# Performance work log

Measured on AMD Instinct MI355X. Metric: run time of the kernel, lower is better.

## Reference

```python
import jax, jax.numpy as jnp
import numpy as np

N_NODES = 40000
N_EDGES = 640000
N_FEAT = 128
HIDDEN = 128
N_GRAPHS = 64


def _sage_conv(x, src, dst, Wl, b, Wr):
    # PyG SAGEConv (aggr='mean', root_weight=True, normalize=False):
    # out_i = W_l @ mean_{j in N(i)} x_j + b + W_r @ x_i
    msg = x[src]                                             # [E, F]
    s = jax.ops.segment_sum(msg, dst, num_segments=N_NODES)  # [N, F]
    deg = jax.ops.segment_sum(jnp.ones((src.shape[0],), x.dtype), dst,
                              num_segments=N_NODES)
    agg = s / jnp.maximum(deg, 1.0)[:, None]
    return agg @ Wl + b + x @ Wr


def setup_inputs() -> dict:
    key = jax.random.key(0)
    ks = jax.random.split(key, 12)
    sc = 1.0 / np.sqrt(N_FEAT)
    x = jax.random.normal(ks[0], (N_NODES, N_FEAT), dtype=jnp.float32)
    edge_index = jax.random.randint(ks[1], (2, N_EDGES), 0, N_NODES, dtype=jnp.int32)
    batch = jnp.sort(jax.random.randint(ks[2], (N_NODES,), 0, N_GRAPHS, dtype=jnp.int32))
    mk = lambda k, shp: (jax.random.normal(k, shp, dtype=jnp.float32) * sc)
    return {
        'x': x, 'edge_index': edge_index, 'batch': batch,
        'W1l': mk(ks[3], (N_FEAT, HIDDEN)), 'b1': jnp.zeros((HIDDEN,), jnp.float32),
        'W1r': mk(ks[4], (N_FEAT, HIDDEN)),
        'W2l': mk(ks[5], (HIDDEN, HIDDEN)), 'b2': jnp.zeros((HIDDEN,), jnp.float32),
        'W2r': mk(ks[6], (HIDDEN, HIDDEN)),
        'W3l': mk(ks[7], (HIDDEN, HIDDEN)), 'b3': jnp.zeros((HIDDEN,), jnp.float32),
        'W3r': mk(ks[8], (HIDDEN, HIDDEN)),
        'Wlin': mk(ks[9], (3 * HIDDEN, HIDDEN)), 'blin': jnp.zeros((HIDDEN,), jnp.float32),
    }


def reference(x, edge_index, batch, W1l, b1, W1r, W2l, b2, W2r, W3l, b3, W3r, Wlin, blin):
    src, dst = edge_index[0], edge_index[1]
    h1 = jax.nn.relu(_sage_conv(x, src, dst, W1l, b1, W1r))
    h2 = jax.nn.relu(_sage_conv(h1, src, dst, W2l, b2, W2r))
    h3 = jax.nn.relu(_sage_conv(h2, src, dst, W3l, b3, W3r))
    h = jnp.concatenate([h1, h2, h3], axis=1)                # [N, 3*H]
    pooled = jax.ops.segment_sum(h, batch, num_segments=N_GRAPHS)  # global_add_pool
    out = jax.nn.relu(pooled @ Wlin + blin)                  # [G, H]
    return out
```

## Files before the change

kernel.cpp:

```cpp
#include <hip/hip_runtime.h>
#include <hip/hip_bf16.h>

#define N_NODES 40000
#define N_EDGES 640000
#define NFEAT 128
#define NGRAPHS 64
#define ECAP 1024


typedef __attribute__((ext_vector_type(8))) short short8;
typedef __attribute__((ext_vector_type(4))) float float4v;
typedef __attribute__((ext_vector_type(2))) float float2v;

static __device__ __forceinline__ unsigned short f2bf(float f) {
    unsigned int x = __builtin_bit_cast(unsigned int, f);
    unsigned int r = x + 0x7fffu + ((x >> 16) & 1u);
    return (unsigned short)(r >> 16);
}

__global__ void k_prep(const int* __restrict__ dst, int* __restrict__ deg,
                       const float* __restrict__ x, unsigned short* __restrict__ h0,
                       const float* __restrict__ Wl0, const float* __restrict__ Wr0,
                       const float* __restrict__ Wl1, const float* __restrict__ Wr1,
                       const float* __restrict__ Wl2, const float* __restrict__ Wr2,
                       unsigned short* __restrict__ Wt, float* __restrict__ pooled) {
    int b = blockIdx.x;
    if (b < 625) {
        int e0 = b * 1024 + threadIdx.x;
        #pragma unroll
        for (int k = 0; k < 4; ++k) {
            int e = e0 + k * 256;
            if (e < N_EDGES) atomicAdd(&deg[dst[e]], 1);
        }
    } else if (b < 1875) {
        const int n = N_NODES * NFEAT / 8;
        int i0 = (b - 625) * 512 + threadIdx.x;
        const float4* xf = (const float4*)x;
        #pragma unroll
        for (int k = 0; k < 2; ++k) {
            int i = i0 + k * 256;
            if (i < n) {
                float4 p0 = xf[2 * i], p1 = xf[2 * i + 1];
                uint4 v;
                v.x = (unsigned int)f2bf(p0.x) | ((unsigned int)f2bf(p0.y) << 16);
                v.y = (unsigned int)f2bf(p0.z) | ((unsigned int)f2bf(p0.w) << 16);
                v.z = (unsigned int)f2bf(p1.x) | ((unsigned int)f2bf(p1.y) << 16);
                v.w = (unsigned int)f2bf(p1.z) | ((unsigned int)f2bf(p1.w) << 16);
                ((uint4*)h0)[i] = v;
            }
        }
    } else if (b < 2259) {
        int id = (b - 1875) * 256 + threadIdx.x;
        if (id >= 3 * 128 * 256) return;
        int l   = id >> 15;
        int rem = id & 32767;
        int nn  = rem >> 8;
        int k   = rem & 255;
        const float* Wl = (l == 0) ? Wl0 : (l == 1) ? Wl1 : Wl2;
        const float* Wr = (l == 0) ? Wr0 : (l == 1) ? Wr1 : Wr2;
        float v = (k < 128) ? Wl[k * 128 + nn] : Wr[(k - 128) * 128 + nn];
        Wt[id] = f2bf(v);
    } else {
        int j = (b - 2259) * 256 + threadIdx.x;
        if (j < NGRAPHS * 384) pooled[j] = 0.f;
    }
}

__global__ __launch_bounds__(1024) void k_scan(const int* __restrict__ deg,
                                               int* __restrict__ offsets,
                                               int* __restrict__ cursor) {
    __shared__ int ws[16];
    __shared__ int s_boff;
    int tid = threadIdx.x;
    int b = blockIdx.x;
    int lane = tid & 63, wave = tid >> 6;

    int lim = b << 10;
    int s = 0;
    for (int i = tid; i < lim; i += 1024) s += deg[i];
    for (int d = 1; d < 64; d <<= 1) s += __shfl_xor(s, d, 64);
    if (lane == 0) ws[wave] = s;
    __syncthreads();
    if (tid == 0) {
        int t = 0;
        for (int w = 0; w < 16; ++w) t += ws[w];
        s_boff = t;
    }
    __syncthreads();
    int boff = s_boff;

    int i = (b << 10) + tid;
    int v = (i < N_NODES) ? deg[i] : 0;
    int incl = v;
    for (int d = 1; d < 64; d <<= 1) {
        int t = __shfl_up(incl, d, 64);
        if (lane >= d) incl += t;
    }
    __syncthreads();
    if (lane == 63) ws[wave] = incl;
    __syncthreads();
    if (wave == 0 && lane < 16) {
        int w = ws[lane];
        for (int d = 1; d < 16; d <<= 1) {
            int t = __shfl_up(w, d, 64);
            if (lane >= d) w += t;
        }
        ws[lane] = w;
    }
    __syncthreads();
    int waveOff = (wave == 0) ? 0 : ws[wave - 1];
    if (i < N_NODES) {
        int o = boff + waveOff + incl - v;
        offsets[i] = o;
        cursor[i]  = o;
    }
    if (b == 39 && tid == 0) offsets[N_NODES] = N_EDGES;
}

__global__ void k_fill(const int* __restrict__ src, const int* __restrict__ dst,
                       int* __restrict__ cursor, unsigned short* __restrict__ esrc) {
    int e0 = blockIdx.x * 512 + threadIdx.x;
    #pragma unroll
    for (int k = 0; k < 2; ++k) {
        int e = e0 + k * 256;
        if (e < N_EDGES) {
            int d = dst[e];
            int p = atomicAdd(&cursor[d], 1);
            esrc[p] = (unsigned short)src[e];
        }
    }
}

__global__ __launch_bounds__(256, 8) void k_sage(
        const unsigned short* __restrict__ hin,
        const int* __restrict__ offsets,
        const unsigned short* __restrict__ esrc,
        const int* __restrict__ batch,
        const unsigned short* __restrict__ Wt,
        const float* __restrict__ bias,
        unsigned short* __restrict__ hout,
        float* __restrict__ poolseg) {
    __shared__ __align__(16) unsigned short As[32][264];
    __shared__ __align__(16) unsigned short eidx[ECAP];
    int tid = threadIdx.x;
    int row0 = blockIdx.x * 32;

    int estart = offsets[row0];
    int ecnt   = offsets[row0 + 32] - estart;
    int staged = ecnt < ECAP ? ecnt : ECAP;

    for (int p = 0; p < 2; ++p) {
        int ci = tid + p * 256;
        int r = ci >> 4, c8 = ci & 15;
        uint4 v = *(const uint4*)(hin + (size_t)(row0 + r) * 128 + c8 * 8);
        *(uint4*)(&As[r][128 + c8 * 8]) = v;
    }
    for (int t = tid; t < staged; t += 256) eidx[t] = esrc[estart + t];
    __syncthreads();

    {
        int grp = tid >> 4;
        int sub = tid & 15;
        for (int nn = 0; nn < 2; ++nn) {
            int r = nn * 16 + grp;
            int node = row0 + r;
            int beg = offsets[node], end = offsets[node + 1];
            float2v a0 = {0.f, 0.f}, a1 = a0, a2 = a0, a3 = a0;
            auto acc8 = [&](uint4 u) {
                float2v t0, t1, t2, t3;
                t0.x = __builtin_bit_cast(float, u.x << 16);
                t0.y = __builtin_bit_cast(float, u.x & 0xffff0000u);
                t1.x = __builtin_bit_cast(float, u.y << 16);
                t1.y = __builtin_bit_cast(float, u.y & 0xffff0000u);
                t2.x = __builtin_bit_cast(float, u.z << 16);
                t2.y = __builtin_bit_cast(float, u.z & 0xffff0000u);
                t3.x = __builtin_bit_cast(float, u.w << 16);
                t3.y = __builtin_bit_cast(float, u.w & 0xffff0000u);
                a0 += t0; a1 += t1; a2 += t2; a3 += t3;
            };
            if (end - estart <= staged) {
                int lj = beg - estart, lend = end - estart;
                for (; lj + 8 <= lend; lj += 8) {
                    int s0 = eidx[lj],     s1 = eidx[lj + 1];
                    int s2 = eidx[lj + 2], s3 = eidx[lj + 3];
                    int s4 = eidx[lj + 4], s5 = eidx[lj + 5];
                    int s6 = eidx[lj + 6], s7 = eidx[lj + 7];
                    uint4 u0 = *(const uint4*)(hin + (size_t)s0 * 128 + sub * 8);
                    uint4 u1 = *(const uint4*)(hin + (size_t)s1 * 128 + sub * 8);
                    uint4 u2 = *(const uint4*)(hin + (size_t)s2 * 128 + sub * 8);
                    uint4 u3 = *(const uint4*)(hin + (size_t)s3 * 128 + sub * 8);
                    uint4 u4 = *(const uint4*)(hin + (size_t)s4 * 128 + sub * 8);
                    uint4 u5 = *(const uint4*)(hin + (size_t)s5 * 128 + sub * 8);
                    uint4 u6 = *(const uint4*)(hin + (size_t)s6 * 128 + sub * 8);
                    uint4 u7 = *(const uint4*)(hin + (size_t)s7 * 128 + sub * 8);
                    acc8(u0); acc8(u1); acc8(u2); acc8(u3);
                    acc8(u4); acc8(u5); acc8(u6); acc8(u7);
                }
                for (; lj < lend; ++lj) {
                    int s = eidx[lj];
                    uint4 u = *(const uint4*)(hin + (size_t)s * 128 + sub * 8);
                    acc8(u);
                }
            } else {
                for (int j = beg; j < end; ++j) {
                    int s = esrc[j];
                    uint4 u = *(const uint4*)(hin + (size_t)s * 128 + sub * 8);
                    acc8(u);
                }
            }
            int deg = end - beg;
            float inv = 1.f / (float)(deg > 1 ? deg : 1);
            uint4 v;
            v.x = (unsigned int)f2bf(a0.x * inv) | ((unsigned int)f2bf(a0.y * inv) << 16);
            v.y = (unsigned int)f2bf(a1.x * inv) | ((unsigned int)f2bf(a1.y * inv) << 16);
            v.z = (unsigned int)f2bf(a2.x * inv) | ((unsigned int)f2bf(a2.y * inv) << 16);
            v.w = (unsigned int)f2bf(a3.x * inv) | ((unsigned int)f2bf(a3.y * inv) << 16);
            *(uint4*)(&As[r][sub * 8]) = v;
        }
    }
    __syncthreads();

    int wave = tid >> 6, lane = tid & 63;
    int quad = lane >> 4, l16 = lane & 15;
    float4v acc[2][2];
    for (int rt = 0; rt < 2; ++rt)
        for (int ct = 0; ct < 2; ++ct) acc[rt][ct] = {0.f, 0.f, 0.f, 0.f};

    int ncol0 = wave * 32;
    for (int kc = 0; kc < 8; ++kc) {
        int k0 = kc * 32 + quad * 8;
        short8 a[2], b[2];
        for (int rt = 0; rt < 2; ++rt)
            a[rt] = *(const short8*)(&As[rt * 16 + l16][k0]);
        for (int ct = 0; ct < 2; ++ct)
            b[ct] = *(const short8*)(Wt + (size_t)(ncol0 + ct * 16 + l16) * 256 + k0);
        for (int rt = 0; rt < 2; ++rt)
            for (int ct = 0; ct < 2; ++ct)
                acc[rt][ct] = __builtin_amdgcn_mfma_f32_16x16x32_bf16(
                    a[rt], b[ct], acc[rt][ct], 0, 0, 0);
    }

    __syncthreads();
    float* Ps = (float*)&As[0][0];
    int* sbatch = (int*)&eidx[0];
    if (tid < 32) sbatch[tid] = batch[row0 + tid];

    for (int ct = 0; ct < 2; ++ct) {
        int col = ncol0 + ct * 16 + l16;
        float bv = bias[col];
        for (int rt = 0; rt < 2; ++rt) {
            int r0 = rt * 16 + quad * 4;
            for (int i = 0; i < 4; ++i) {
                float v = acc[rt][ct][i] + bv;
                v = v > 0.f ? v : 0.f;
                if (hout) hout[(size_t)(row0 + r0 + i) * 128 + col] = f2bf(v);
                Ps[(r0 + i) * 132 + col] = v;
            }
        }
    }
    __syncthreads();

    {
        int half = tid >> 7;
        int c = tid & 127;
        int rbase = half * 16;
        float accp = 0.f;
        int cur = sbatch[rbase];
        for (int r = rbase; r < rbase + 16; ++r) {
            int g = sbatch[r];
            if (g != cur) {
                atomicAdd(&poolseg[cur * 384 + c], accp);
                accp = 0.f;
                cur = g;
            }
            accp += Ps[r * 132 + c];
        }
        atomicAdd(&poolseg[cur * 384 + c], accp);
    }
}

__global__ void k_final(const float* __restrict__ pooled,
                        const float* __restrict__ Wlin,
                        const float* __restrict__ blin,
                        float* __restrict__ out) {
    __shared__ float part[128];
    int g = blockIdx.x;
    int t = threadIdx.x;
    int col = t & 127, half = t >> 7;
    int k0 = half * 192;
    float acc = 0.f;
    for (int k = k0; k < k0 + 192; ++k)
        acc = fmaf(pooled[g * 384 + k], Wlin[k * 128 + col], acc);
    if (half) part[col] = acc;
    __syncthreads();
    if (!half) {
        float v = acc + part[col] + blin[col];
        out[g * 128 + col] = v > 0.f ? v : 0.f;
    }
}

extern "C" void kernel_launch(void* const* d_in, const int* in_sizes, int n_in,
                              void* d_out, int out_size, void* d_ws, size_t ws_size,
                              hipStream_t stream) {
    const float* x    = (const float*)d_in[0];
    const int*   ei   = (const int*)d_in[1];
    const int*   src  = ei;
    const int*   dst  = ei + N_EDGES;
    const int*   batch = (const int*)d_in[2];
    const float* W1l = (const float*)d_in[3];
    const float* b1  = (const float*)d_in[4];
    const float* W1r = (const float*)d_in[5];
    const float* W2l = (const float*)d_in[6];
    const float* b2  = (const float*)d_in[7];
    const float* W2r = (const float*)d_in[8];
    const float* W3l = (const float*)d_in[9];
    const float* b3  = (const float*)d_in[10];
    const float* W3r = (const float*)d_in[11];
    const float* Wlin = (const float*)d_in[12];
    const float* blin = (const float*)d_in[13];
    float* out = (float*)d_out;

    char* ws = (char*)d_ws;
    size_t off = 0;
    auto alloc = [&](size_t bytes) -> char* {
        char* p = ws + off;
        off = (off + bytes + 255) & ~(size_t)255;
        return p;
    };
    int* offsets = (int*)alloc((N_NODES + 1) * sizeof(int));
    int* cursor  = (int*)alloc(N_NODES * sizeof(int));
    int* deg     = (int*)alloc(N_NODES * sizeof(int));
    unsigned short* esrc = (unsigned short*)alloc(N_EDGES * sizeof(unsigned short));
    unsigned short* h0   = (unsigned short*)alloc((size_t)N_NODES * 128 * 2);
    unsigned short* h1   = (unsigned short*)alloc((size_t)N_NODES * 128 * 2);
    unsigned short* h2   = (unsigned short*)alloc((size_t)N_NODES * 128 * 2);
    unsigned short* Wt   = (unsigned short*)alloc(3 * 256 * 128 * 2);
    float* pooled = (float*)alloc(NGRAPHS * 384 * sizeof(float));

    hipMemsetAsync(deg, 0, N_NODES * sizeof(int), stream);

    k_prep<<<2355, 256, 0, stream>>>(dst, deg, x, h0,
                                     W1l, W1r, W2l, W2r, W3l, W3r, Wt, pooled);
    k_scan<<<40, 1024, 0, stream>>>(deg, offsets, cursor);
    k_fill<<<1250, 256, 0, stream>>>(src, dst, cursor, esrc);

    k_sage<<<1250, 256, 0, stream>>>(h0, offsets, esrc, batch, Wt,
                                     b1, h1, pooled);
    k_sage<<<1250, 256, 0, stream>>>(h1, offsets, esrc, batch, Wt + 32768,
                                     b2, h2, pooled + 128);
    k_sage<<<1250, 256, 0, stream>>>(h2, offsets, esrc, batch, Wt + 2 * 32768,
                                     b3, (unsigned short*)nullptr, pooled + 256);

    k_final<<<NGRAPHS, 256, 0, stream>>>(pooled, Wlin, blin, out);
}
```

Measured before the change: 257.1 us.

## Double-buffer neighbor gathers with masked 8-wide batches in SAGE aggregation

Restructures the neighbor-mean gather loop so two 8-edge batches are kept in flight at once: the next batch's loads are issued before the current batch is accumulated. Tails are handled by clamping indices and masking with a 0/1 multiplier via FMA, which removes the scalar remainder loop. Launch bounds are relaxed from 8 to 4 blocks per SM to give room for the extra registers the two 8-wide uint4 buffers need. The trade-off is lower occupancy and some redundant loads on tail batches, in exchange for more memory-level parallelism per thread.

```diff
diff --git a/kernel.cpp b/kernel.cpp
--- a/kernel.cpp
+++ b/kernel.cpp
@@ -131,7 +131,7 @@
     }
 }
 
-__global__ __launch_bounds__(256, 8) void k_sage(
+__global__ __launch_bounds__(256, 4) void k_sage(
         const unsigned short* __restrict__ hin,
         const int* __restrict__ offsets,
         const unsigned short* __restrict__ esrc,
@@ -161,12 +161,14 @@
     {
         int grp = tid >> 4;
         int sub = tid & 15;
+        const unsigned short* hsub = hin + sub * 8;
         for (int nn = 0; nn < 2; ++nn) {
             int r = nn * 16 + grp;
             int node = row0 + r;
             int beg = offsets[node], end = offsets[node + 1];
             float2v a0 = {0.f, 0.f}, a1 = a0, a2 = a0, a3 = a0;
-            auto acc8 = [&](uint4 u) {
+            auto acc1 = [&](uint4 u, float m) {
+                float2v mv = {m, m};
                 float2v t0, t1, t2, t3;
                 t0.x = __builtin_bit_cast(float, u.x << 16);
                 t0.y = __builtin_bit_cast(float, u.x & 0xffff0000u);
@@ -176,36 +178,65 @@
                 t2.y = __builtin_bit_cast(float, u.z & 0xffff0000u);
                 t3.x = __builtin_bit_cast(float, u.w << 16);
                 t3.y = __builtin_bit_cast(float, u.w & 0xffff0000u);
-                a0 += t0; a1 += t1; a2 += t2; a3 += t3;
+                a0 = t0 * mv + a0;
+                a1 = t1 * mv + a1;
+                a2 = t2 * mv + a2;
+                a3 = t3 * mv + a3;
+            };
+            auto accb = [&](const uint4* U, int rem) {
+                #pragma unroll
+                for (int i = 0; i < 8; ++i)
+                    acc1(U[i], i < rem ? 1.f : 0.f);
             };
             if (end - estart <= staged) {
                 int lj = beg - estart, lend = end - estart;
-                for (; lj + 8 <= lend; lj += 8) {
-                    int s0 = eidx[lj],     s1 = eidx[lj + 1];
-                    int s2 = eidx[lj + 2], s3 = eidx[lj + 3];
-                    int s4 = eidx[lj + 4], s5 = eidx[lj + 5];
-                    int s6 = eidx[lj + 6], s7 = eidx[lj + 7];
-                    uint4 u0 = *(const uint4*)(hin + (size_t)s0 * 128 + sub * 8);
-                    uint4 u1 = *(const uint4*)(hin + (size_t)s1 * 128 + sub * 8);
-                    uint4 u2 = *(const uint4*)(hin + (size_t)s2 * 128 + sub * 8);
-                    uint4 u3 = *(const uint4*)(hin + (size_t)s3 * 128 + sub * 8);
-                    uint4 u4 = *(const uint4*)(hin + (size_t)s4 * 128 + sub * 8);
-                    uint4 u5 = *(const uint4*)(hin + (size_t)s5 * 128 + sub * 8);
-                    uint4 u6 = *(const uint4*)(hin + (size_t)s6 * 128 + sub * 8);
-                    uint4 u7 = *(const uint4*)(hin + (size_t)s7 * 128 + sub * 8);
-                    acc8(u0); acc8(u1); acc8(u2); acc8(u3);
-                    acc8(u4); acc8(u5); acc8(u6); acc8(u7);
-                }
-                for (; lj < lend; ++lj) {
-                    int s = eidx[lj];
-                    uint4 u = *(const uint4*)(hin + (size_t)s * 128 + sub * 8);
-                    acc8(u);
+                int len = lend - lj;
+                if (len > 0) {
+                    int jmax = lend - 1;
+                    auto issue = [&](int base, uint4* U) {
+                        #pragma unroll
+                        for (int i = 0; i < 8; ++i) {
+                            int j = base + i;
+                            j = j <= jmax ? j : jmax;
+                            int s = eidx[j];
+                            U[i] = *(const uint4*)(hsub + (size_t)s * 128);
+                        }
+                    };
+                    uint4 U[8], V[8];
+                    issue(lj, U);
+                    int remU = len;
+                    int b = lj + 8;
+                    while (b < lend) {
+                        issue(b, V);
+                        accb(U, remU);
+                        int remV = lend - b;
+                        b += 8;
+                        if (b < lend) {
+                            issue(b, U);
+                            accb(V, remV);
+                            remU = lend - b;
+                            b += 8;
+                        } else {
+                            accb(V, remV);
+                            remU = 0;
+                            break;
+                        }
+                    }
+                    if (remU > 0) accb(U, remU);
                 }
             } else {
-                for (int j = beg; j < end; ++j) {
-                    int s = esrc[j];
-                    uint4 u = *(const uint4*)(hin + (size_t)s * 128 + sub * 8);
-                    acc8(u);
+                int jmax = end - 1;
+                for (int j = beg; j < end; j += 8) {
+                    int rem = end - j;
+                    uint4 U[8];
+                    #pragma unroll
+                    for (int i = 0; i < 8; ++i) {
+                        int jj = j + i;
+                        jj = jj <= jmax ? jj : jmax;
+                        int s = esrc[jj];
+                        U[i] = *(const uint4*)(hsub + (size_t)s * 128);
+                    }
+                    accb(U, rem);
                 }
             }
             int deg = end - beg;
```

New measurement: 262.3 us. 1.02x slower.

## Stage neighbor rows into LDS with async double-buffered global_load_lds

Applied to the files above, without the earlier changes.

Replaces the per-thread register gather of neighbor feature rows with a block-cooperative, double-buffered pipeline. The whole block stages 64 edges' bf16 rows at a time into LDS using global_load_lds, while the previously staged chunk is accumulated from LDS. The goal is to keep many gather loads in flight and hide their latency. In exchange it adds about 32KB of LDS, two barriers per chunk, and some wasted loads (clamped slots at the tail). Occupancy is lowered (launch bounds 8→4), and nodes with skewed degrees now wait on each other at block barriers.

```diff
diff --git a/kernel.cpp b/kernel.cpp
--- a/kernel.cpp
+++ b/kernel.cpp
@@ -6,6 +6,7 @@
 #define NFEAT 128
 #define NGRAPHS 64
 #define ECAP 1024
+#define CHUNK 64
 
 
 typedef __attribute__((ext_vector_type(8))) short short8;
@@ -16,6 +17,13 @@
     unsigned int x = __builtin_bit_cast(unsigned int, f);
     unsigned int r = x + 0x7fffu + ((x >> 16) & 1u);
     return (unsigned short)(r >> 16);
+}
+
+static __device__ __forceinline__ void stage16(const unsigned short* g,
+                                               unsigned short* l) {
+    __builtin_amdgcn_global_load_lds(
+        (const __attribute__((address_space(1))) void*)g,
+        (__attribute__((address_space(3))) void*)l, 16, 0, 0);
 }
 
 __global__ void k_prep(const int* __restrict__ dst, int* __restrict__ deg,
@@ -131,7 +139,7 @@
     }
 }
 
-__global__ __launch_bounds__(256, 8) void k_sage(
+__global__ __launch_bounds__(256, 4) void k_sage(
         const unsigned short* __restrict__ hin,
         const int* __restrict__ offsets,
         const unsigned short* __restrict__ esrc,
@@ -141,13 +149,14 @@
         unsigned short* __restrict__ hout,
         float* __restrict__ poolseg) {
     __shared__ __align__(16) unsigned short As[32][264];
+    __shared__ __align__(16) unsigned short Ebuf[2][CHUNK * 128];
     __shared__ __align__(16) unsigned short eidx[ECAP];
     int tid = threadIdx.x;
     int row0 = blockIdx.x * 32;
 
     int estart = offsets[row0];
     int ecnt   = offsets[row0 + 32] - estart;
-    int staged = ecnt < ECAP ? ecnt : ECAP;
+    int SC = ecnt < ECAP ? ecnt : ECAP;
 
     for (int p = 0; p < 2; ++p) {
         int ci = tid + p * 256;
@@ -155,72 +164,114 @@
         uint4 v = *(const uint4*)(hin + (size_t)(row0 + r) * 128 + c8 * 8);
         *(uint4*)(&As[r][128 + c8 * 8]) = v;
     }
-    for (int t = tid; t < staged; t += 256) eidx[t] = esrc[estart + t];
-    __syncthreads();
-
+    for (int t = tid; t < SC; t += 256) eidx[t] = esrc[estart + t];
+    __syncthreads();
+
+    int lane = tid & 63, wave = tid >> 6;
+    int grp = tid >> 4, sub = tid & 15;
+
+    int beg0, end0, beg1, end1;
     {
-        int grp = tid >> 4;
-        int sub = tid & 15;
-        for (int nn = 0; nn < 2; ++nn) {
-            int r = nn * 16 + grp;
-            int node = row0 + r;
-            int beg = offsets[node], end = offsets[node + 1];
-            float2v a0 = {0.f, 0.f}, a1 = a0, a2 = a0, a3 = a0;
-            auto acc8 = [&](uint4 u) {
-                float2v t0, t1, t2, t3;
-                t0.x = __builtin_bit_cast(float, u.x << 16);
-                t0.y = __builtin_bit_cast(float, u.x & 0xffff0000u);
-                t1.x = __builtin_bit_cast(float, u.y << 16);
-                t1.y = __builtin_bit_cast(float, u.y & 0xffff0000u);
-                t2.x = __builtin_bit_cast(float, u.z << 16);
-                t2.y = __builtin_bit_cast(float, u.z & 0xffff0000u);
-                t3.x = __builtin_bit_cast(float, u.w << 16);
-                t3.y = __builtin_bit_cast(float, u.w & 0xffff0000u);
-                a0 += t0; a1 += t1; a2 += t2; a3 += t3;
-            };
-            if (end - estart <= staged) {
-                int lj = beg - estart, lend = end - estart;
-                for (; lj + 8 <= lend; lj += 8) {
-                    int s0 = eidx[lj],     s1 = eidx[lj + 1];
-                    int s2 = eidx[lj + 2], s3 = eidx[lj + 3];
-                    int s4 = eidx[lj + 4], s5 = eidx[lj + 5];
-                    int s6 = eidx[lj + 6], s7 = eidx[lj + 7];
-                    uint4 u0 = *(const uint4*)(hin + (size_t)s0 * 128 + sub * 8);
-                    uint4 u1 = *(const uint4*)(hin + (size_t)s1 * 128 + sub * 8);
-                    uint4 u2 = *(const uint4*)(hin + (size_t)s2 * 128 + sub * 8);
-                    uint4 u3 = *(const uint4*)(hin + (size_t)s3 * 128 + sub * 8);
-                    uint4 u4 = *(const uint4*)(hin + (size_t)s4 * 128 + sub * 8);
-                    uint4 u5 = *(const uint4*)(hin + (size_t)s5 * 128 + sub * 8);
-                    uint4 u6 = *(const uint4*)(hin + (size_t)s6 * 128 + sub * 8);
-                    uint4 u7 = *(const uint4*)(hin + (size_t)s7 * 128 + sub * 8);
-                    acc8(u0); acc8(u1); acc8(u2); acc8(u3);
-                    acc8(u4); acc8(u5); acc8(u6); acc8(u7);
-                }
-                for (; lj < lend; ++lj) {
-                    int s = eidx[lj];
-                    uint4 u = *(const uint4*)(hin + (size_t)s * 128 + sub * 8);
-                    acc8(u);
-                }
+        int n0 = row0 + grp,      n1 = row0 + 16 + grp;
+        beg0 = offsets[n0] - estart;  end0 = offsets[n0 + 1] - estart;
+        beg1 = offsets[n1] - estart;  end1 = offsets[n1 + 1] - estart;
+    }
+    float2v A0[4], A1[4];
+    #pragma unroll
+    for (int i = 0; i < 4; ++i) { A0[i] = {0.f, 0.f}; A1[i] = {0.f, 0.f}; }
+
+    auto addu = [&](uint4 u, float2v* A) {
+        float2v t0, t1, t2, t3;
+        t0.x = __builtin_bit_cast(float, u.x << 16);
+        t0.y = __builtin_bit_cast(float, u.x & 0xffff0000u);
+        t1.x = __builtin_bit_cast(float, u.y << 16);
+        t1.y = __builtin_bit_cast(float, u.y & 0xffff0000u);
+        t2.x = __builtin_bit_cast(float, u.z << 16);
+        t2.y = __builtin_bit_cast(float, u.z & 0xffff0000u);
+        t3.x = __builtin_bit_cast(float, u.w << 16);
+        t3.y = __builtin_bit_cast(float, u.w & 0xffff0000u);
+        A[0] += t0; A[1] += t1; A[2] += t2; A[3] += t3;
+    };
+
+    int nc = (SC + CHUNK - 1) >> 6;
+    if (nc > 0) {
+        auto stage_chunk = [&](int c, int par) {
+            int c0 = c << 6;
+            #pragma unroll
+            for (int i = 0; i < 4; ++i) {
+                int slot = wave * 4 + i;
+                int el = c0 + slot * 4 + (lane >> 4);
+                el = el < SC - 1 ? el : SC - 1;
+                int s = eidx[el];
+                const unsigned short* g = hin + (size_t)s * 128 + (lane & 15) * 8;
+                stage16(g, &Ebuf[par][slot * 512]);
+            }
+        };
+        auto accum_chunk = [&](int c, int par) {
+            int c0 = c << 6, c1 = c0 + CHUNK;
+            int lim = c1 < SC ? c1 : SC;
+            {
+                int lo = beg0 > c0 ? beg0 : c0;
+                int hi = end0 < lim ? end0 : lim;
+                for (int e = lo; e < hi; ++e)
+                    addu(*(const uint4*)&Ebuf[par][(e - c0) * 128 + sub * 8], A0);
+            }
+            {
+                int lo = beg1 > c0 ? beg1 : c0;
+                int hi = end1 < lim ? end1 : lim;
+                for (int e = lo; e < hi; ++e)
+                    addu(*(const uint4*)&Ebuf[par][(e - c0) * 128 + sub * 8], A1);
+            }
+        };
+
+        stage_chunk(0, 0);
+        for (int c = 0; c < nc; ++c) {
+            int par = c & 1;
+            if (c + 1 < nc) {
+                stage_chunk(c + 1, par ^ 1);
+                asm volatile("s_waitcnt vmcnt(4)" ::: "memory");
             } else {
-                for (int j = beg; j < end; ++j) {
-                    int s = esrc[j];
-                    uint4 u = *(const uint4*)(hin + (size_t)s * 128 + sub * 8);
-                    acc8(u);
-                }
-            }
-            int deg = end - beg;
-            float inv = 1.f / (float)(deg > 1 ? deg : 1);
-            uint4 v;
-            v.x = (unsigned int)f2bf(a0.x * inv) | ((unsigned int)f2bf(a0.y * inv) << 16);
-            v.y = (unsigned int)f2bf(a1.x * inv) | ((unsigned int)f2bf(a1.y * inv) << 16);
-            v.z = (unsigned int)f2bf(a2.x * inv) | ((unsigned int)f2bf(a2.y * inv) << 16);
-            v.w = (unsigned int)f2bf(a3.x * inv) | ((unsigned int)f2bf(a3.y * inv) << 16);
-            *(uint4*)(&As[r][sub * 8]) = v;
-        }
-    }
-    __syncthreads();
-
-    int wave = tid >> 6, lane = tid & 63;
+                asm volatile("s_waitcnt vmcnt(0)" ::: "memory");
+            }
+            __builtin_amdgcn_sched_barrier(0);
+            __builtin_amdgcn_s_barrier();
+            __builtin_amdgcn_sched_barrier(0);
+            accum_chunk(c, par);
+            __builtin_amdgcn_sched_barrier(0);
+            __builtin_amdgcn_s_barrier();
+        }
+    }
+    if (ecnt > SC) {
+        for (int e = (beg0 > SC ? beg0 : SC); e < end0; ++e) {
+            int s = esrc[estart + e];
+            addu(*(const uint4*)(hin + (size_t)s * 128 + sub * 8), A0);
+        }
+        for (int e = (beg1 > SC ? beg1 : SC); e < end1; ++e) {
+            int s = esrc[estart + e];
+            addu(*(const uint4*)(hin + (size_t)s * 128 + sub * 8), A1);
+        }
+    }
+
+    {
+        int d0 = end0 - beg0;
+        float inv0 = 1.f / (float)(d0 > 1 ? d0 : 1);
+        uint4 v;
+        v.x = (unsigned int)f2bf(A0[0].x * inv0) | ((unsigned int)f2bf(A0[0].y * inv0) << 16);
+        v.y = (unsigned int)f2bf(A0[1].x * inv0) | ((unsigned int)f2bf(A0[1].y * inv0) << 16);
+        v.z = (unsigned int)f2bf(A0[2].x * inv0) | ((unsigned int)f2bf(A0[2].y * inv0) << 16);
+        v.w = (unsigned int)f2bf(A0[3].x * inv0) | ((unsigned int)f2bf(A0[3].y * inv0) << 16);
+        *(uint4*)(&As[grp][sub * 8]) = v;
+        int d1 = end1 - beg1;
+        float inv1 = 1.f / (float)(d1 > 1 ? d1 : 1);
+        uint4 w;
+        w.x = (unsigned int)f2bf(A1[0].x * inv1) | ((unsigned int)f2bf(A1[0].y * inv1) << 16);
+        w.y = (unsigned int)f2bf(A1[1].x * inv1) | ((unsigned int)f2bf(A1[1].y * inv1) << 16);
+        w.z = (unsigned int)f2bf(A1[2].x * inv1) | ((unsigned int)f2bf(A1[2].y * inv1) << 16);
+        w.w = (unsigned int)f2bf(A1[3].x * inv1) | ((unsigned int)f2bf(A1[3].y * inv1) << 16);
+        *(uint4*)(&As[16 + grp][sub * 8]) = w;
+    }
+    __syncthreads();
+
     int quad = lane >> 4, l16 = lane & 15;
     float4v acc[2][2];
     for (int rt = 0; rt < 2; ++rt)
```

After: 323.6 us. +25.9%, slower.
